# Kernel optimization log

Hardware: AMD Instinct MI355X
Metric: run time of the kernel (lower is better)

The kernel has to match this reference:

```python
import jax, jax.numpy as jnp
import numpy as np
import math

B, L, D, H = 4, 2048, 1024, 16
HD = D // H  # head dim = 64


def setup_inputs() -> dict:
    key = jax.random.key(0)
    ks = jax.random.split(key, 5)
    s = 1.0 / math.sqrt(D)
    return {
        "x": jax.random.normal(ks[0], (B, L, D), dtype=jnp.float32),
        "Wqkv": jax.random.normal(ks[1], (D, 3 * D), dtype=jnp.float32) * s,
        "bqkv": jax.random.normal(ks[2], (3 * D,), dtype=jnp.float32) * 0.02,
        "Wproj": jax.random.normal(ks[3], (D, D), dtype=jnp.float32) * s,
        "bproj": jax.random.normal(ks[4], (D,), dtype=jnp.float32) * 0.02,
    }


def reference(x, Wqkv, bqkv, Wproj, bproj):
    Bsz, Ls, Ds = x.shape
    qkv = x @ Wqkv + bqkv                     # [B, L, 3D]
    q, k, v = jnp.split(qkv, 3, axis=-1)      # each [B, L, D]

    def heads(t):  # [B, L, D] -> [B, H, L, HD]
        return t.reshape(Bsz, Ls, H, HD).transpose(0, 2, 1, 3)

    q, k, v = heads(q), heads(k), heads(v)
    att = jnp.einsum("bhqd,bhkd->bhqk", q, k) / jnp.sqrt(jnp.float32(HD))
    causal = jnp.tril(jnp.ones((Ls, Ls), dtype=bool))
    att = jnp.where(causal[None, None], att, -jnp.inf)
    att = jax.nn.softmax(att, axis=-1)
    y = jnp.einsum("bhqk,bhkd->bhqd", att, v)  # [B, H, L, HD]
    y = y.transpose(0, 2, 1, 3).reshape(Bsz, Ls, Ds)
    return y @ Wproj + bproj
```

## Files before the change

### kernel.cpp

```cpp
#include <hip/hip_runtime.h>


typedef __bf16 bf16x2 __attribute__((ext_vector_type(2)));
typedef __bf16 bf16x4 __attribute__((ext_vector_type(4)));
typedef __bf16 bf16x8 __attribute__((ext_vector_type(8)));
typedef float f32x4 __attribute__((ext_vector_type(4)));
typedef float f32x16 __attribute__((ext_vector_type(16)));
typedef unsigned u32x4 __attribute__((ext_vector_type(4)));

#define MFMA16(a, b, c) __builtin_amdgcn_mfma_f32_16x16x32_bf16(a, b, c, 0, 0, 0)
#define MFMA32(a, b, c) __builtin_amdgcn_mfma_f32_32x32x16_bf16(a, b, c, 0, 0, 0)

__device__ __forceinline__ void gload_lds16(const __bf16* g, __bf16* l) {
    __builtin_amdgcn_global_load_lds(
        (const __attribute__((address_space(1))) void*)g,
        (__attribute__((address_space(3))) void*)l, 16, 0, 0);
}

__device__ __forceinline__ unsigned pkbf(float a, float b) {
    bf16x2 t = {(__bf16)a, (__bf16)b};
    return __builtin_bit_cast(unsigned, t);
}

__global__ void fused_convert_kernel(const float* __restrict__ x, __bf16* __restrict__ xb,
                                     const float* __restrict__ wqkv, __bf16* __restrict__ wqkvT,
                                     const float* __restrict__ wproj, __bf16* __restrict__ wprojT)
{
    const int blk = blockIdx.x;
    if (blk < 4096) {
        int i = (blk * 256 + threadIdx.x) * 8;
        f32x4 lo = *(const f32x4*)&x[i];
        f32x4 hi = *(const f32x4*)&x[i + 4];
        bf16x8 o;
#pragma unroll
        for (int j = 0; j < 4; ++j) { o[j] = (__bf16)lo[j]; o[j + 4] = (__bf16)hi[j]; }
        *(bf16x8*)&xb[i] = o;
        return;
    }
    __shared__ __bf16 t[32][33];
    const float* in;
    __bf16* out;
    int R, C, bx, by;
    if (blk < 7168) {
        int b2 = blk - 4096;
        bx = b2 % 96; by = b2 / 96; in = wqkv; out = wqkvT; R = 1024; C = 3072;
    } else {
        int b2 = blk - 7168;
        bx = b2 % 32; by = b2 / 32; in = wproj; out = wprojT; R = 1024; C = 1024;
    }
    const int c0 = bx * 32, r0 = by * 32;
    const int tx = threadIdx.x & 31, ty = threadIdx.x >> 5;
#pragma unroll
    for (int j = 0; j < 4; ++j) {
        int r = ty + j * 8;
        t[tx][r] = (__bf16)in[(size_t)(r0 + r) * C + c0 + tx];
    }
    __syncthreads();
#pragma unroll
    for (int j = 0; j < 4; ++j) {
        int r = ty + j * 8;
        out[(size_t)(c0 + r) * R + r0 + tx] = t[r][tx];
    }
}

#define GEMM_TILE_LOOP(Abase, Bbase)                                               \
    for (int k0 = 0; k0 < 1024; k0 += 64) {                                        \
        __syncthreads();                                                           \
        _Pragma("unroll")                                                          \
        for (int l = 0; l < 4; ++l) {                                              \
            int base = l * 256 + w * 64;                                           \
            int r = (base >> 3) + (lane >> 3);                                     \
            int c = (lane & 7) ^ (r & 7);                                          \
            gload_lds16(&Abase[(size_t)(m0 + r) * 1024 + k0 + c * 8], &As[base * 8]); \
            gload_lds16(&Bbase[(size_t)(n0 + r) * 1024 + k0 + c * 8], &Bs[base * 8]); \
        }                                                                          \
        __syncthreads();                                                           \
        bf16x8 af[2][4], bfr[2][4];                                                \
        _Pragma("unroll")                                                          \
        for (int kk = 0; kk < 2; ++kk) {                                           \
            _Pragma("unroll")                                                      \
            for (int mf = 0; mf < 4; ++mf) {                                       \
                int rr = wr * 64 + mf * 16 + row;                                  \
                af[kk][mf] = *(const bf16x8*)                                      \
                    &As[rr * 64 + (((kk * 4 + g) ^ (rr & 7)) * 8)];                \
            }                                                                      \
            _Pragma("unroll")                                                      \
            for (int nf = 0; nf < 4; ++nf) {                                       \
                int rr = wc * 64 + nf * 16 + row;                                  \
                bfr[kk][nf] = *(const bf16x8*)                                     \
                    &Bs[rr * 64 + (((kk * 4 + g) ^ (rr & 7)) * 8)];                \
            }                                                                      \
        }                                                                          \
        _Pragma("unroll")                                                          \
        for (int kk = 0; kk < 2; ++kk)                                             \
            _Pragma("unroll")                                                      \
            for (int mf = 0; mf < 4; ++mf)                                         \
                _Pragma("unroll")                                                  \
                for (int nf = 0; nf < 4; ++nf)                                     \
                    acc[mf][nf] = MFMA16(af[kk][mf], bfr[kk][nf], acc[mf][nf]);    \
    }

__global__ __launch_bounds__(256, 2)
void qkv_gemm_kernel(const __bf16* __restrict__ A, const __bf16* __restrict__ Bt,
                     const float* __restrict__ bias,
                     __bf16* __restrict__ q2, __bf16* __restrict__ k2,
                     __bf16* __restrict__ v2)
{
    __shared__ __bf16 stage[16384];
    __bf16* const As = stage;
    __bf16* const Bs = stage + 8192;
    const int tid = threadIdx.x;
    const int lane = tid & 63;
    const int w = tid >> 6;
    const int wr = w >> 1, wc = w & 1;
    const int row = lane & 15, g = lane >> 4;
    const int m0 = blockIdx.x * 128;
    const int n0 = blockIdx.y * 128;

    const f32x4 fzero = {0.f, 0.f, 0.f, 0.f};
    f32x4 acc[4][4];
#pragma unroll
    for (int a = 0; a < 4; ++a)
#pragma unroll
        for (int b = 0; b < 4; ++b) acc[a][b] = fzero;

    GEMM_TILE_LOOP(A, Bt)

    __syncthreads();
    const int part = n0 >> 10;
    const float QSCL = 0.18033688f;
    if (part == 2) {
#pragma unroll
        for (int mf = 0; mf < 4; ++mf)
#pragma unroll
            for (int nf = 0; nf < 4; ++nf) {
                int nl = nf * 16 + row;
                float bv = bias[n0 + wc * 64 + nl];
                bf16x4 pv;
#pragma unroll
                for (int i = 0; i < 4; ++i)
                    pv[i] = (__bf16)(acc[mf][nf][i] + bv);
                int c = (mf >> 1) * 4 + (nl >> 5) * 2 + (mf & 1);
                int off0 = (g & 1) * 256 + (nl & 31) * 8 + ((g >> 1) & 1) * 4;
                *(unsigned long long*)&stage[w * 4096 + c * 512 + off0] =
                    __builtin_bit_cast(unsigned long long, pv);
            }
    } else {
#pragma unroll
        for (int mf = 0; mf < 4; ++mf)
#pragma unroll
            for (int nf = 0; nf < 4; ++nf) {
                int nl = nf * 16 + row;
                float bv = bias[n0 + wc * 64 + nl];
#pragma unroll
                for (int i = 0; i < 4; ++i) {
                    int ml = mf * 16 + g * 4 + i;
                    float fv = acc[mf][nf][i] + bv;
                    if (part == 0) fv *= QSCL;
                    int c = (ml >> 5) * 4 + (nl >> 4);
                    int off = ((nl >> 3) & 1) * 256 + (ml & 31) * 8 + (nl & 7);
                    stage[w * 4096 + c * 512 + off] = (__bf16)fv;
                }
            }
    }
    {
        const int b = m0 >> 11;
        const int lbase5 = (m0 & 2047) >> 5;
        const int hh = ((n0 & 1023) >> 6) + wc;
        const size_t bh64 = (size_t)(b * 16 + hh) * 64;
        __bf16* dst = part == 0 ? q2 : (part == 1 ? k2 : v2);
#pragma unroll
        for (int c = 0; c < 8; ++c) {
            bf16x8 val = *(const bf16x8*)&stage[w * 4096 + c * 512 + lane * 8];
            size_t gbase = ((bh64 + lbase5 + wr * 2 + (c >> 2)) * 4 + (c & 3)) * 512;
            *(bf16x8*)&dst[gbase + lane * 8] = val;
        }
    }
}

__global__ __launch_bounds__(256, 2)
void proj_gemm_kernel(const __bf16* __restrict__ A, const __bf16* __restrict__ Bt,
                      const float* __restrict__ bias, float* __restrict__ out)
{
    __shared__ __bf16 As[128 * 64];
    __shared__ __bf16 Bs[128 * 64];
    const int tid = threadIdx.x;
    const int lane = tid & 63;
    const int w = tid >> 6;
    const int wr = w >> 1, wc = w & 1;
    const int row = lane & 15, g = lane >> 4;
    const int m0 = blockIdx.x * 128;
    const int n0 = blockIdx.y * 128;

    const f32x4 fzero = {0.f, 0.f, 0.f, 0.f};
    f32x4 acc[4][4];
#pragma unroll
    for (int a = 0; a < 4; ++a)
#pragma unroll
        for (int b = 0; b < 4; ++b) acc[a][b] = fzero;

    GEMM_TILE_LOOP(A, Bt)

#pragma unroll
    for (int mf = 0; mf < 4; ++mf)
#pragma unroll
        for (int nf = 0; nf < 4; ++nf) {
            int n = n0 + wc * 64 + nf * 16 + row;
            float bv = bias[n];
#pragma unroll
            for (int i = 0; i < 4; ++i) {
                int mm = m0 + wr * 64 + mf * 16 + g * 4 + i;
                out[(size_t)mm * 1024 + n] = acc[mf][nf][i] + bv;
            }
        }
}

__global__ __launch_bounds__(128, 2)
void attn_kernel(const __bf16* __restrict__ Q2, const __bf16* __restrict__ K2,
                 const __bf16* __restrict__ V2, __bf16* __restrict__ Yw)
{
    const int tid = threadIdx.x;
    const int lane = tid & 63;
    const int wv = tid >> 6;
    const int col = lane & 31;
    const int hi = lane >> 5;
    const int i0 = blockIdx.x;
    const int bh = (i0 & 7) * 8 + ((i0 >> 3) & 7);
    const int t = (i0 >> 6) * 2 + wv;
    const int tB = 63 - t;
    const int qA = t * 32;
    const int qB = tB * 32;
    const size_t tb = (size_t)bh * 64;

    bf16x8 qfA[4], qfB[4];
#pragma unroll
    for (int dc = 0; dc < 4; ++dc) {
        qfA[dc] = *(const bf16x8*)&Q2[((tb + t) * 4 + dc) * 512 + lane * 8];
        qfB[dc] = *(const bf16x8*)&Q2[((tb + tB) * 4 + dc) * 512 + lane * 8];
    }

    bf16x8 ones;
#pragma unroll
    for (int j = 0; j < 8; ++j) ones[j] = (__bf16)1.0f;

    f32x16 CZ;
#pragma unroll
    for (int i = 0; i < 16; ++i) CZ[i] = 0.f;

    f32x16 OtA[2], OtB[2], OsA, OsB;
#pragma unroll
    for (int dt = 0; dt < 2; ++dt)
#pragma unroll
        for (int i = 0; i < 16; ++i) { OtA[dt][i] = 0.f; OtB[dt][i] = 0.f; }
#pragma unroll
    for (int i = 0; i < 16; ++i) { OsA[i] = 0.f; OsB[i] = 0.f; }

    auto smxpack = [&](f32x16& st, f32x16& Os, bool diag,
                       bf16x8& pa0, bf16x8& pa1) {
        if (diag) {
#pragma unroll
            for (int r = 0; r < 16; ++r) {
                int crow = (r & 3) + 8 * (r >> 2) + 4 * hi;
                if (crow > col) st[r] = -1e30f;
            }
        }
#pragma unroll
        for (int r = 0; r < 16; ++r) st[r] = exp2f(st[r]);
        u32x4 w0 = {pkbf(st[0], st[1]), pkbf(st[2], st[3]),
                    pkbf(st[4], st[5]), pkbf(st[6], st[7])};
        u32x4 w1 = {pkbf(st[8], st[9]), pkbf(st[10], st[11]),
                    pkbf(st[12], st[13]), pkbf(st[14], st[15])};
        pa0 = __builtin_bit_cast(bf16x8, w0);
        pa1 = __builtin_bit_cast(bf16x8, w1);
        Os = MFMA32(ones, pa0, Os);
        Os = MFMA32(ones, pa1, Os);
    };

    const __bf16* kp = K2 + tb * 2048 + lane * 8;
    const __bf16* vp = V2 + tb * 2048 + lane * 8;

    bf16x8 kfP[4], vfP[4];
#pragma unroll
    for (int dc = 0; dc < 4; ++dc) {
        kfP[dc] = *(const bf16x8*)&kp[dc * 512];
        vfP[dc] = *(const bf16x8*)&vp[dc * 512];
    }

    const int nsteps = tB + 1;
    for (int kt = 0; kt < nsteps; ++kt) {
        const bool dual = (kt <= t);
        const __bf16* kpn = kp + 2048;
        const __bf16* vpn = vp + 2048;
        bf16x8 kfQ[4], vfQ[4];
#pragma unroll
        for (int dc = 0; dc < 4; ++dc) {
            kfQ[dc] = *(const bf16x8*)&kpn[dc * 512];
            vfQ[dc] = *(const bf16x8*)&vpn[dc * 512];
        }

        f32x16 stA, stB;
        __builtin_amdgcn_s_setprio(1);
        stB = MFMA32(kfP[0], qfB[0], CZ);
        stB = MFMA32(kfP[1], qfB[1], stB);
        stB = MFMA32(kfP[2], qfB[2], stB);
        stB = MFMA32(kfP[3], qfB[3], stB);
        if (dual) {
            stA = MFMA32(kfP[0], qfA[0], CZ);
            stA = MFMA32(kfP[1], qfA[1], stA);
            stA = MFMA32(kfP[2], qfA[2], stA);
            stA = MFMA32(kfP[3], qfA[3], stA);
        }
        __builtin_amdgcn_s_setprio(0);

        bf16x8 paA0, paA1, paB0, paB1;
        smxpack(stB, OsB, kt == tB, paB0, paB1);
        if (dual) smxpack(stA, OsA, kt == t, paA0, paA1);

        __builtin_amdgcn_s_setprio(1);
        OtB[0] = MFMA32(vfP[0], paB0, OtB[0]);
        OtB[0] = MFMA32(vfP[1], paB1, OtB[0]);
        OtB[1] = MFMA32(vfP[2], paB0, OtB[1]);
        OtB[1] = MFMA32(vfP[3], paB1, OtB[1]);
        if (dual) {
            OtA[0] = MFMA32(vfP[0], paA0, OtA[0]);
            OtA[0] = MFMA32(vfP[1], paA1, OtA[0]);
            OtA[1] = MFMA32(vfP[2], paA0, OtA[1]);
            OtA[1] = MFMA32(vfP[3], paA1, OtA[1]);
        }
        __builtin_amdgcn_s_setprio(0);

#pragma unroll
        for (int dc = 0; dc < 4; ++dc) { kfP[dc] = kfQ[dc]; vfP[dc] = vfQ[dc]; }
        kp = kpn; vp = vpn;
    }

    const int b = bh >> 4, h = bh & 15;
    const float invA = 1.f / OsA[0], invB = 1.f / OsB[0];
    __bf16* yrowA = Yw + ((size_t)(b * 2048 + qA + col)) * 1024 + h * 64;
    __bf16* yrowB = Yw + ((size_t)(b * 2048 + qB + col)) * 1024 + h * 64;
#pragma unroll
    for (int dt = 0; dt < 2; ++dt)
#pragma unroll
        for (int rg = 0; rg < 4; ++rg) {
            int d0 = dt * 32 + rg * 8 + hi * 4;
            unsigned lo = pkbf(OtA[dt][rg * 4 + 0] * invA, OtA[dt][rg * 4 + 1] * invA);
            unsigned h2 = pkbf(OtA[dt][rg * 4 + 2] * invA, OtA[dt][rg * 4 + 3] * invA);
            *(unsigned long long*)&yrowA[d0] =
                (unsigned long long)lo | ((unsigned long long)h2 << 32);
            lo = pkbf(OtB[dt][rg * 4 + 0] * invB, OtB[dt][rg * 4 + 1] * invB);
            h2 = pkbf(OtB[dt][rg * 4 + 2] * invB, OtB[dt][rg * 4 + 3] * invB);
            *(unsigned long long*)&yrowB[d0] =
                (unsigned long long)lo | ((unsigned long long)h2 << 32);
        }
}

extern "C" void kernel_launch(void* const* d_in, const int* in_sizes, int n_in,
                              void* d_out, int out_size, void* d_ws, size_t ws_size,
                              hipStream_t stream)
{
    const float* x     = (const float*)d_in[0];
    const float* wqkv  = (const float*)d_in[1];
    const float* bqkv  = (const float*)d_in[2];
    const float* wproj = (const float*)d_in[3];
    const float* bproj = (const float*)d_in[4];
    float* out = (float*)d_out;

    const size_t E = (size_t)4 * 16 * 2048 * 64;
    __bf16* q2     = (__bf16*)d_ws;
    __bf16* k2     = q2 + E;
    __bf16* v2     = k2 + E;
    __bf16* xb     = v2 + E;
    __bf16* y      = xb;
    __bf16* wqkvT  = xb + E;
    __bf16* wprojT = wqkvT + (size_t)3072 * 1024;

    fused_convert_kernel<<<8192, 256, 0, stream>>>(x, xb, wqkv, wqkvT, wproj, wprojT);
    qkv_gemm_kernel<<<dim3(64, 24), 256, 0, stream>>>(xb, wqkvT, bqkv, q2, k2, v2);
    attn_kernel<<<1024, 128, 0, stream>>>(q2, k2, v2, y);
    proj_gemm_kernel<<<dim3(64, 8), 256, 0, stream>>>(y, wprojT, bproj, out);
}
```

Before: 152.7 us.

## Split dual-tile attention waves into single-tile waves with doubled grid

Each attention wave now processes a single 32-row query tile instead of a paired tile (t, 63-t). The two waves in a block still take mirrored tiles, which keeps causal work balanced, and the grid doubles to 2048 blocks. The launch-bounds occupancy hint rises from 2 to 4, and the register prefetch of the next K/V tile is removed. The aim is more resident waves and lower register pressure. The cost is that K/V fragments are no longer shared between two query tiles, so global K/V traffic roughly doubles, and load latency is no longer hidden by the explicit prefetch.

```diff
diff --git a/kernel.cpp b/kernel.cpp
--- a/kernel.cpp
+++ b/kernel.cpp
@@ -215,7 +215,7 @@
         }
 }
 
-__global__ __launch_bounds__(128, 2)
+__global__ __launch_bounds__(128, 4)
 void attn_kernel(const __bf16* __restrict__ Q2, const __bf16* __restrict__ K2,
                  const __bf16* __restrict__ V2, __bf16* __restrict__ Yw)
 {
@@ -226,18 +226,15 @@
     const int hi = lane >> 5;
     const int i0 = blockIdx.x;
     const int bh = (i0 & 7) * 8 + ((i0 >> 3) & 7);
-    const int t = (i0 >> 6) * 2 + wv;
-    const int tB = 63 - t;
-    const int qA = t * 32;
-    const int qB = tB * 32;
+    const int p = i0 >> 6;
+    const int t = wv ? (63 - p) : p;
+    const int qT = t * 32;
     const size_t tb = (size_t)bh * 64;
 
-    bf16x8 qfA[4], qfB[4];
-#pragma unroll
-    for (int dc = 0; dc < 4; ++dc) {
-        qfA[dc] = *(const bf16x8*)&Q2[((tb + t) * 4 + dc) * 512 + lane * 8];
-        qfB[dc] = *(const bf16x8*)&Q2[((tb + tB) * 4 + dc) * 512 + lane * 8];
-    }
+    bf16x8 qf[4];
+#pragma unroll
+    for (int dc = 0; dc < 4; ++dc)
+        qf[dc] = *(const bf16x8*)&Q2[((tb + t) * 4 + dc) * 512 + lane * 8];
 
     bf16x8 ones;
 #pragma unroll
@@ -247,17 +244,34 @@
 #pragma unroll
     for (int i = 0; i < 16; ++i) CZ[i] = 0.f;
 
-    f32x16 OtA[2], OtB[2], OsA, OsB;
+    f32x16 Ot[2], Os;
 #pragma unroll
     for (int dt = 0; dt < 2; ++dt)
 #pragma unroll
-        for (int i = 0; i < 16; ++i) { OtA[dt][i] = 0.f; OtB[dt][i] = 0.f; }
-#pragma unroll
-    for (int i = 0; i < 16; ++i) { OsA[i] = 0.f; OsB[i] = 0.f; }
-
-    auto smxpack = [&](f32x16& st, f32x16& Os, bool diag,
-                       bf16x8& pa0, bf16x8& pa1) {
-        if (diag) {
+        for (int i = 0; i < 16; ++i) Ot[dt][i] = 0.f;
+#pragma unroll
+    for (int i = 0; i < 16; ++i) Os[i] = 0.f;
+
+    const __bf16* kp = K2 + tb * 2048 + lane * 8;
+    const __bf16* vp = V2 + tb * 2048 + lane * 8;
+
+    for (int kt = 0; kt <= t; ++kt) {
+        bf16x8 kf[4], vf[4];
+#pragma unroll
+        for (int dc = 0; dc < 4; ++dc) {
+            kf[dc] = *(const bf16x8*)&kp[dc * 512];
+            vf[dc] = *(const bf16x8*)&vp[dc * 512];
+        }
+
+        f32x16 st;
+        __builtin_amdgcn_s_setprio(1);
+        st = MFMA32(kf[0], qf[0], CZ);
+        st = MFMA32(kf[1], qf[1], st);
+        st = MFMA32(kf[2], qf[2], st);
+        st = MFMA32(kf[3], qf[3], st);
+        __builtin_amdgcn_s_setprio(0);
+
+        if (kt == t) {
 #pragma unroll
             for (int r = 0; r < 16; ++r) {
                 int crow = (r & 3) + 8 * (r >> 2) + 4 * hi;
@@ -270,86 +284,32 @@
                     pkbf(st[4], st[5]), pkbf(st[6], st[7])};
         u32x4 w1 = {pkbf(st[8], st[9]), pkbf(st[10], st[11]),
                     pkbf(st[12], st[13]), pkbf(st[14], st[15])};
-        pa0 = __builtin_bit_cast(bf16x8, w0);
-        pa1 = __builtin_bit_cast(bf16x8, w1);
+        bf16x8 pa0 = __builtin_bit_cast(bf16x8, w0);
+        bf16x8 pa1 = __builtin_bit_cast(bf16x8, w1);
+
+        __builtin_amdgcn_s_setprio(1);
         Os = MFMA32(ones, pa0, Os);
         Os = MFMA32(ones, pa1, Os);
-    };
-
-    const __bf16* kp = K2 + tb * 2048 + lane * 8;
-    const __bf16* vp = V2 + tb * 2048 + lane * 8;
-
-    bf16x8 kfP[4], vfP[4];
-#pragma unroll
-    for (int dc = 0; dc < 4; ++dc) {
-        kfP[dc] = *(const bf16x8*)&kp[dc * 512];
-        vfP[dc] = *(const bf16x8*)&vp[dc * 512];
-    }
-
-    const int nsteps = tB + 1;
-    for (int kt = 0; kt < nsteps; ++kt) {
-        const bool dual = (kt <= t);
-        const __bf16* kpn = kp + 2048;
-        const __bf16* vpn = vp + 2048;
-        bf16x8 kfQ[4], vfQ[4];
-#pragma unroll
-        for (int dc = 0; dc < 4; ++dc) {
-            kfQ[dc] = *(const bf16x8*)&kpn[dc * 512];
-            vfQ[dc] = *(const bf16x8*)&vpn[dc * 512];
-        }
-
-        f32x16 stA, stB;
-        __builtin_amdgcn_s_setprio(1);
-        stB = MFMA32(kfP[0], qfB[0], CZ);
-        stB = MFMA32(kfP[1], qfB[1], stB);
-        stB = MFMA32(kfP[2], qfB[2], stB);
-        stB = MFMA32(kfP[3], qfB[3], stB);
-        if (dual) {
-            stA = MFMA32(kfP[0], qfA[0], CZ);
-            stA = MFMA32(kfP[1], qfA[1], stA);
-            stA = MFMA32(kfP[2], qfA[2], stA);
-            stA = MFMA32(kfP[3], qfA[3], stA);
-        }
+        Ot[0] = MFMA32(vf[0], pa0, Ot[0]);
+        Ot[0] = MFMA32(vf[1], pa1, Ot[0]);
+        Ot[1] = MFMA32(vf[2], pa0, Ot[1]);
+        Ot[1] = MFMA32(vf[3], pa1, Ot[1]);
         __builtin_amdgcn_s_setprio(0);
 
-        bf16x8 paA0, paA1, paB0, paB1;
-        smxpack(stB, OsB, kt == tB, paB0, paB1);
-        if (dual) smxpack(stA, OsA, kt == t, paA0, paA1);
-
-        __builtin_amdgcn_s_setprio(1);
-        OtB[0] = MFMA32(vfP[0], paB0, OtB[0]);
-        OtB[0] = MFMA32(vfP[1], paB1, OtB[0]);
-        OtB[1] = MFMA32(vfP[2], paB0, OtB[1]);
-        OtB[1] = MFMA32(vfP[3], paB1, OtB[1]);
-        if (dual) {
-            OtA[0] = MFMA32(vfP[0], paA0, OtA[0]);
-            OtA[0] = MFMA32(vfP[1], paA1, OtA[0]);
-            OtA[1] = MFMA32(vfP[2], paA0, OtA[1]);
-            OtA[1] = MFMA32(vfP[3], paA1, OtA[1]);
-        }
-        __builtin_amdgcn_s_setprio(0);
-
-#pragma unroll
-        for (int dc = 0; dc < 4; ++dc) { kfP[dc] = kfQ[dc]; vfP[dc] = vfQ[dc]; }
-        kp = kpn; vp = vpn;
+        kp += 2048; vp += 2048;
     }
 
     const int b = bh >> 4, h = bh & 15;
-    const float invA = 1.f / OsA[0], invB = 1.f / OsB[0];
-    __bf16* yrowA = Yw + ((size_t)(b * 2048 + qA + col)) * 1024 + h * 64;
-    __bf16* yrowB = Yw + ((size_t)(b * 2048 + qB + col)) * 1024 + h * 64;
+    const float inv = 1.f / Os[0];
+    __bf16* yrow = Yw + ((size_t)(b * 2048 + qT + col)) * 1024 + h * 64;
 #pragma unroll
     for (int dt = 0; dt < 2; ++dt)
 #pragma unroll
         for (int rg = 0; rg < 4; ++rg) {
             int d0 = dt * 32 + rg * 8 + hi * 4;
-            unsigned lo = pkbf(OtA[dt][rg * 4 + 0] * invA, OtA[dt][rg * 4 + 1] * invA);
-            unsigned h2 = pkbf(OtA[dt][rg * 4 + 2] * invA, OtA[dt][rg * 4 + 3] * invA);
-            *(unsigned long long*)&yrowA[d0] =
-                (unsigned long long)lo | ((unsigned long long)h2 << 32);
-            lo = pkbf(OtB[dt][rg * 4 + 0] * invB, OtB[dt][rg * 4 + 1] * invB);
-            h2 = pkbf(OtB[dt][rg * 4 + 2] * invB, OtB[dt][rg * 4 + 3] * invB);
-            *(unsigned long long*)&yrowB[d0] =
+            unsigned lo = pkbf(Ot[dt][rg * 4 + 0] * inv, Ot[dt][rg * 4 + 1] * inv);
+            unsigned h2 = pkbf(Ot[dt][rg * 4 + 2] * inv, Ot[dt][rg * 4 + 3] * inv);
+            *(unsigned long long*)&yrow[d0] =
                 (unsigned long long)lo | ((unsigned long long)h2 << 32);
         }
 }
@@ -376,6 +336,6 @@
 
     fused_convert_kernel<<<8192, 256, 0, stream>>>(x, xb, wqkv, wqkvT, wproj, wprojT);
     qkv_gemm_kernel<<<dim3(64, 24), 256, 0, stream>>>(xb, wqkvT, bqkv, q2, k2, v2);
-    attn_kernel<<<1024, 128, 0, stream>>>(q2, k2, v2, y);
+    attn_kernel<<<2048, 128, 0, stream>>>(q2, k2, v2, y);
     proj_gemm_kernel<<<dim3(64, 8), 256, 0, stream>>>(y, wprojT, bproj, out);
 }
```

New measurement: 154.6 us. Within noise of the previous version (+1.2%).
